# Performance work log

Measured on AMD Instinct MI355X. Metric: run time of the kernel, lower is better.

Reference implementation:

```python
import jax, jax.numpy as jnp
import numpy as np

LO = 30            # rollout horizon (hard-coded in SimCore)
AS_DIM = 400       # ssbm_actionstate_dim
HEAD = AS_DIM + 7  # per-player decoder width


def setup_inputs() -> dict:
    key = jax.random.key(0)
    ks = jax.random.split(key, 12)
    T, B, A, H = 128, 256, 64, 1024
    Nt, Ng = 6, 4
    Lu = T - 1 - LO
    s = 0.02
    return dict(
        observations=jax.random.uniform(ks[0], (T, B, 16), jnp.float32),
        actions=jax.random.normal(ks[1], (T, B, A), jnp.float32),
        beliefs=jax.random.normal(ks[2], (T, B, H), jnp.float32),
        w_ih=jax.random.normal(ks[3], (3 * H, A), jnp.float32) * s,
        w_hh=jax.random.normal(ks[4], (3 * H, H), jnp.float32) * s,
        b_ih=jnp.zeros((3 * H,), jnp.float32),
        b_hh=jnp.zeros((3 * H,), jnp.float32),
        pre_w1=jax.random.normal(ks[5], (64, H), jnp.float32) * s,
        pre_b1=jnp.zeros((64,), jnp.float32),
        pre_w2=jax.random.normal(ks[6], (H, 64), jnp.float32) * s,
        pre_b2=jnp.zeros((H,), jnp.float32),
        dec_w=jax.random.normal(ks[7], (2 * HEAD, H), jnp.float32) * s,
        dec_b=jnp.zeros((2 * HEAD,), jnp.float32),
        idx_i=jax.random.randint(ks[8], (Nt,), 0, Lu, dtype=jnp.int32),
        K=jax.random.randint(ks[9], (Nt, Ng), 0, LO, dtype=jnp.int32),
    )


def _bce_logits(x, t):
    # binary_cross_entropy_with_logits, elementwise
    return jax.nn.softplus(x) - x * t


def _player_loss(pred, tgt):
    # pred: [Nt,Ng,B,407] logits; tgt: [Nt,Ng,B,8] observation half
    # pytorch means are over everything except the Nt python loop -> mean over (Ng,B[,feat])
    logits = pred[..., :AS_DIM]
    cls = tgt[..., 0].astype(jnp.int32)                     # .long() of float target
    ce = -jnp.take_along_axis(jax.nn.log_softmax(logits, -1), cls[..., None], -1)[..., 0]
    loss = ce.mean(axis=(1, 2))
    loss = loss + ((pred[..., 400:402] - tgt[..., 1:3]) ** 2).mean(axis=(1, 2, 3))
    loss = loss + ((jax.nn.softplus(pred[..., 402:403]) - tgt[..., 3:4]) ** 2).mean(axis=(1, 2, 3))
    loss = loss + ((jax.nn.softplus(pred[..., 403:404]) - tgt[..., 4:5]) ** 2).mean(axis=(1, 2, 3))
    loss = loss + _bce_logits(pred[..., 404:405], tgt[..., 5:6]).mean(axis=(1, 2, 3))
    loss = loss + _bce_logits(pred[..., 405:406], tgt[..., 6:7]).mean(axis=(1, 2, 3))
    loss = loss + _bce_logits(pred[..., 406:407], tgt[..., 7:8]).mean(axis=(1, 2, 3))
    return loss  # [Nt]


def reference(observations, actions, beliefs, w_ih, w_hh, b_ih, b_hh,
              pre_w1, pre_b1, pre_w2, pre_b2, dec_w, dec_b, idx_i, K):
    def gru_cell(h, a):
        gi = a @ w_ih.T + b_ih              # [B,3H]
        gh = h @ w_hh.T + b_hh
        ir, iz, in_ = jnp.split(gi, 3, axis=-1)
        hr, hz, hn = jnp.split(gh, 3, axis=-1)
        r = jax.nn.sigmoid(ir + hr)
        z = jax.nn.sigmoid(iz + hz)
        n = jnp.tanh(in_ + r * hn)
        h_new = (1.0 - z) * n + z * h
        return h_new, h_new

    def rollout(i, k):
        h0 = beliefs[i]                                          # [B,H]
        acts = jax.lax.dynamic_slice_in_dim(actions, i, LO, axis=0)
        _, states = jax.lax.scan(gru_cell, h0, acts)             # [Lo,B,H]
        return states[k], observations[k + i + 1]                # [Ng,B,H],[Ng,B,16]

    states, obs = jax.vmap(rollout)(idx_i, K)                    # [Nt,Ng,B,H]

    # ResidualBlock: x + relu(relu(x W1^T + b1) W2^T + b2)
    h = jax.nn.relu(states @ pre_w1.T + pre_b1)
    x = states + jax.nn.relu(h @ pre_w2.T + pre_b2)

    logits = x @ dec_w.T + dec_b                                 # [Nt,Ng,B,814]
    agent, opponent = logits[..., :HEAD], logits[..., HEAD:]
    tgt_a, tgt_o = obs[..., :8], obs[..., 8:]

    loss = (_player_loss(agent, tgt_a) + _player_loss(opponent, tgt_o)).sum()
    return loss
```

## Files before the change

kernel.cpp:

```cpp
#include <hip/hip_runtime.h>
#include <hip/hip_bf16.h>
#include <hip/hip_fp8.h>

typedef __bf16 bf16;
typedef unsigned char u8;
typedef __attribute__((ext_vector_type(4))) __bf16 bf16x4;
typedef __attribute__((ext_vector_type(8))) __bf16 bf16x8;
typedef __attribute__((ext_vector_type(4))) float f32x4;

static __device__ __forceinline__ f32x4 MFMA16(bf16x8 a, bf16x8 b, f32x4 c) {
  return __builtin_amdgcn_mfma_f32_16x16x32_bf16(a, b, c, 0, 0, 0);
}
static __device__ __forceinline__ f32x4 MFMA8(long a, long b, f32x4 c) {
  return __builtin_amdgcn_mfma_f32_16x16x32_fp8_fp8(a, b, c, 0, 0, 0);
}

__device__ __forceinline__ float sigm(float x) { return 1.0f / (1.0f + __expf(-x)); }
__device__ __forceinline__ float softplus_(float x) {
  return fmaxf(x, 0.0f) + log1pf(__expf(-fabsf(x)));
}
__device__ __forceinline__ u8 to_fp8(float x) {
  __hip_fp8_e4m3 v(x);
  return (u8)v.__x;
}

__device__ __forceinline__ void gl16(const void* g, char* l) {
  __builtin_amdgcn_global_load_lds(
      (const __attribute__((address_space(1))) char*)g,
      (__attribute__((address_space(3))) char*)l, 16, 0, 0);
}

__global__ void k_prep(const float* __restrict__ whh, const float* __restrict__ wih,
                       const float* __restrict__ act, const float* __restrict__ w1,
                       const float* __restrict__ w2, const float* __restrict__ dw,
                       const float* __restrict__ beliefs, const int* __restrict__ idx_i,
                       u8* __restrict__ Wh8, bf16* __restrict__ Wib,
                       bf16* __restrict__ actb, bf16* __restrict__ w1b,
                       bf16* __restrict__ w2b, bf16* __restrict__ dwb,
                       bf16* __restrict__ hA, u8* __restrict__ hA8) {
  for (int q = blockIdx.x * blockDim.x + threadIdx.x; q < 1994240;
       q += gridDim.x * blockDim.x) {
    if (q < 814592) {
      const float* src;
      bf16* dst;
      int off;
      if (q < 49152)       { src = wih; dst = Wib;  off = q; }
      else if (q < 573440) { src = act; dst = actb; off = q - 49152; }
      else if (q < 589824) { src = w1;  dst = w1b;  off = q - 573440; }
      else if (q < 606208) { src = w2;  dst = w2b;  off = q - 589824; }
      else                 { src = dw;  dst = dwb;  off = q - 606208; }
      float4 v = *(const float4*)&src[(size_t)off << 2];
      bf16x4 o = {(bf16)v.x, (bf16)v.y, (bf16)v.z, (bf16)v.w};
      *(bf16x4*)&dst[(size_t)off << 2] = o;
    } else if (q < 1207808) {
      const int e = (q - 814592) << 2;
      const int n = e >> 18, rest = e & 262143;
      float4 v = *(const float4*)&beliefs[((size_t)idx_i[n] << 18) + rest];
      bf16x4 o = {(bf16)v.x, (bf16)v.y, (bf16)v.z, (bf16)v.w};
      *(bf16x4*)&hA[e] = o;
      unsigned w = (unsigned)to_fp8(v.x) | ((unsigned)to_fp8(v.y) << 8) |
                   ((unsigned)to_fp8(v.z) << 16) | ((unsigned)to_fp8(v.w) << 24);
      *(unsigned*)&hA8[e] = w;
    } else {
      const int off = q - 1207808;
      float4 v = *(const float4*)&whh[(size_t)off << 2];
      unsigned w = (unsigned)to_fp8(v.x) | ((unsigned)to_fp8(v.y) << 8) |
                   ((unsigned)to_fp8(v.z) << 16) | ((unsigned)to_fp8(v.w) << 24);
      *(unsigned*)&Wh8[(size_t)off << 2] = w;
    }
  }
}

__global__ __launch_bounds__(256, 2) void k_gru_step(
    const bf16* __restrict__ hin, const u8* __restrict__ hin8,
    bf16* __restrict__ hout, u8* __restrict__ hout8,
    const u8* __restrict__ Wh8, const bf16* __restrict__ Wib,
    const bf16* __restrict__ actb,
    const float* __restrict__ b_ih, const float* __restrict__ b_hh,
    const int* __restrict__ idx_i, const int* __restrict__ Kmat,
    bf16* __restrict__ states, int step) {
  const int pid = blockIdx.x;
  const int xcd = pid & 7;
  const int rg = xcd >> 2;
  const int cgp = xcd & 3;
  const int q = pid >> 3;
  const int mtl = q & 7;
  const int jtl = q >> 3;
  const int m0 = rg * 768 + mtl * 96;
  const int j0 = (cgp * 8 + jtl) * 32;

  {
    const int nlo = m0 >> 8, nhi = (m0 + 95) >> 8;
    int mk = max(max(Kmat[nlo * 4 + 0], Kmat[nlo * 4 + 1]),
                 max(Kmat[nlo * 4 + 2], Kmat[nlo * 4 + 3]));
    if (nhi != nlo)
      mk = max(mk, max(max(Kmat[nhi * 4 + 0], Kmat[nhi * 4 + 1]),
                       max(Kmat[nhi * 4 + 2], Kmat[nhi * 4 + 3])));
    if (step > mk) return;
  }

  const int tid = threadIdx.x, wave = tid >> 6, lane = tid & 63;
  const int l15 = lane & 15;
  const int kgrp = lane >> 4;
  const int wm = wave >> 1;
  const int wj = wave & 1;
  const int jlane = j0 + wj * 16 + l15;

  __shared__ alignas(16) char As[3 * 12288];
  __shared__ alignas(16) char Bs[3 * 12288];

  const int srow = lane >> 3;
  int a8off[3], b8off[3], aioff[3], bioff[3];
#pragma unroll
  for (int i = 0; i < 3; ++i) {
    const int r = wave * 24 + i * 8 + srow;
    const int grow = m0 + r;
    a8off[i] = grow * 1024 + ((((lane & 7) ^ ((r >> 1) & 7)) << 4));
    const int wr = (r >> 5) * 1024 + j0 + (r & 31);
    b8off[i] = wr * 1024 + ((((lane & 7) ^ ((r >> 1) & 7)) << 4));
    const int scol = (((lane & 7) ^ srow) << 3);
    const int np = grow >> 8;
    aioff[i] = ((idx_i[np] + step) * 256 + (grow & 255)) * 64 + scol;
    bioff[i] = wr * 64 + scol;
  }

  auto stage = [&](int buf, int slot) {
    char* ad = As + buf * 12288 + (wave * 24) * 128;
    char* bd = Bs + buf * 12288 + (wave * 24) * 128;
    if (slot < 8) {
#pragma unroll
      for (int i = 0; i < 3; ++i) {
        gl16(hin8 + a8off[i] + slot * 128, ad + i * 1024);
        gl16(Wh8 + b8off[i] + slot * 128, bd + i * 1024);
      }
    } else {
#pragma unroll
      for (int i = 0; i < 3; ++i) {
        gl16(actb + aioff[i], ad + i * 1024);
        gl16(Wib + bioff[i], bd + i * 1024);
      }
    }
  };

  f32x4 accR[3], accZ[3], accNh[3], accNi[3];
  const f32x4 zero = {0.f, 0.f, 0.f, 0.f};
#pragma unroll
  for (int f = 0; f < 3; ++f) { accR[f] = zero; accZ[f] = zero; accNh[f] = zero; accNi[f] = zero; }

  const float br = b_ih[jlane] + b_hh[jlane];
  const float bz = b_ih[1024 + jlane] + b_hh[1024 + jlane];
  const float bin = b_ih[2048 + jlane];
  const float bhn = b_hh[2048 + jlane];

  const int keyA = ((wm * 48 + l15) >> 1) & 7;
  const int keyB = ((wj * 16 + l15) >> 1) & 7;

  auto computeF8 = [&](int buf) {
    const char* ab = As + buf * 12288;
    const char* bb = Bs + buf * 12288;
    const int ra = wm * 48 + l15;
    const int rb = wj * 16 + l15;
#pragma unroll
    for (int kkI = 0; kkI < 4; ++kkI) {
      const int hi = kkI * 2 + (kgrp >> 1);
      const int lo = (kgrp & 1) << 3;
      const int offA = (((hi ^ keyA) << 4) | lo);
      const int offB = (((hi ^ keyB) << 4) | lo);
      long a0 = *(const long*)(ab + ra * 128 + offA);
      long a1 = *(const long*)(ab + (ra + 16) * 128 + offA);
      long a2 = *(const long*)(ab + (ra + 32) * 128 + offA);
      long b0 = *(const long*)(bb + rb * 128 + offB);
      long b1 = *(const long*)(bb + (rb + 32) * 128 + offB);
      long b2 = *(const long*)(bb + (rb + 64) * 128 + offB);
      accR[0] = MFMA8(a0, b0, accR[0]);
      accR[1] = MFMA8(a1, b0, accR[1]);
      accR[2] = MFMA8(a2, b0, accR[2]);
      accZ[0] = MFMA8(a0, b1, accZ[0]);
      accZ[1] = MFMA8(a1, b1, accZ[1]);
      accZ[2] = MFMA8(a2, b1, accZ[2]);
      accNh[0] = MFMA8(a0, b2, accNh[0]);
      accNh[1] = MFMA8(a1, b2, accNh[1]);
      accNh[2] = MFMA8(a2, b2, accNh[2]);
    }
  };

  auto computeGi = [&]() {
    const char* ab = As + 2 * 12288;
    const char* bb = Bs + 2 * 12288;
#pragma unroll
    for (int kkI = 0; kkI < 2; ++kkI) {
      const int kbyte = (((kkI << 5) + (kgrp << 3)) << 1) ^ ((l15 & 7) << 4);
      bf16x8 a0 = *(const bf16x8*)(ab + (wm * 48 + l15) * 128 + kbyte);
      bf16x8 a1 = *(const bf16x8*)(ab + (wm * 48 + 16 + l15) * 128 + kbyte);
      bf16x8 a2 = *(const bf16x8*)(ab + (wm * 48 + 32 + l15) * 128 + kbyte);
      bf16x8 b_r = *(const bf16x8*)(bb + (wj * 16 + l15) * 128 + kbyte);
      bf16x8 b_z = *(const bf16x8*)(bb + (32 + wj * 16 + l15) * 128 + kbyte);
      bf16x8 b_n = *(const bf16x8*)(bb + (64 + wj * 16 + l15) * 128 + kbyte);
      accR[0] = MFMA16(a0, b_r, accR[0]);
      accR[1] = MFMA16(a1, b_r, accR[1]);
      accR[2] = MFMA16(a2, b_r, accR[2]);
      accZ[0] = MFMA16(a0, b_z, accZ[0]);
      accZ[1] = MFMA16(a1, b_z, accZ[1]);
      accZ[2] = MFMA16(a2, b_z, accZ[2]);
      accNi[0] = MFMA16(a0, b_n, accNi[0]);
      accNi[1] = MFMA16(a1, b_n, accNi[1]);
      accNi[2] = MFMA16(a2, b_n, accNi[2]);
    }
  };

  stage(0, 0);
  stage(1, 1);

  uint2 hpreg[3];

#pragma unroll
  for (int t = 0; t < 9; ++t) {
    if (t < 7) stage((t + 2) % 3, t + 2);
    if (t == 6) {
#pragma unroll
      for (int it2 = 0; it2 < 3; ++it2) {
        const int u = it2 * 256 + tid;
        const int row = u >> 3, c = u & 7;
        hpreg[it2] = *(const uint2*)(hin + (size_t)(m0 + row) * 1024 + j0 + c * 4);
      }
    }
    if (t <= 5)       asm volatile("s_waitcnt vmcnt(12)" ::: "memory");
    else if (t == 6)  asm volatile("s_waitcnt vmcnt(15)" ::: "memory");
    else if (t == 7)  asm volatile("s_waitcnt vmcnt(9)" ::: "memory");
    else              asm volatile("s_waitcnt vmcnt(3)" ::: "memory");
    __builtin_amdgcn_s_barrier();
    if (t == 8) computeGi();
    else        computeF8(t % 3);
    __builtin_amdgcn_sched_barrier(0);
    __builtin_amdgcn_s_barrier();
  }

  asm volatile("s_waitcnt vmcnt(0)" ::: "memory");
  bf16* Hp = (bf16*)As;
  bf16* Hn = (bf16*)Bs;
  u8* Hn8 = (u8*)(As + 12288);

#pragma unroll
  for (int it2 = 0; it2 < 3; ++it2) {
    const int u = it2 * 256 + tid;
    const int row = u >> 3, c = u & 7;
    *(uint2*)&Hp[row * 40 + c * 4] = hpreg[it2];
  }
  __syncthreads();

#pragma unroll
  for (int mf = 0; mf < 3; ++mf) {
#pragma unroll
    for (int ii = 0; ii < 4; ++ii) {
      const int ml = wm * 48 + mf * 16 + kgrp * 4 + ii;
      const int jl = wj * 16 + l15;
      float hp = (float)Hp[ml * 40 + jl];
      float rg2 = sigm(accR[mf][ii] + br);
      float zg = sigm(accZ[mf][ii] + bz);
      float ng = tanhf(accNi[mf][ii] + bin + rg2 * (accNh[mf][ii] + bhn));
      float hnew = (1.0f - zg) * ng + zg * hp;
      Hn[ml * 40 + jl] = (bf16)hnew;
      Hn8[ml * 40 + jl] = to_fp8(hnew);
    }
  }
  __syncthreads();

#pragma unroll
  for (int it2 = 0; it2 < 3; ++it2) {
    const int u = it2 * 256 + tid;
    const int row = u >> 3, c = u & 7;
    const int m = m0 + row;
    uint2 v = *(const uint2*)&Hn[row * 40 + c * 4];
    *(uint2*)&hout[(size_t)m * 1024 + j0 + c * 4] = v;
    if (c < 8) {
    }
    const int n = m >> 8;
    const int b = m & 255;
#pragma unroll
    for (int g = 0; g < 4; ++g) {
      if (Kmat[n * 4 + g] == step)
        *(uint2*)&states[((size_t)(n * 4 + g) * 256 + b) * 1024 + j0 + c * 4] = v;
    }
  }
#pragma unroll
  for (int it2 = 0; it2 < 3; ++it2) {
    const int u = it2 * 256 + tid;
    const int row = u >> 3, c = u & 7;
    *(unsigned*)&hout8[(size_t)(m0 + row) * 1024 + j0 + c * 4] =
        *(const unsigned*)&Hn8[row * 40 + c * 4];
  }
}

template <int EPI, int SWZ>
__global__ __launch_bounds__(256) void k_gemm_epi(
    const bf16* __restrict__ A, const bf16* __restrict__ W, int K, int Nreal, int ld_out,
    const float* __restrict__ bias, const bf16* __restrict__ resid,
    float* __restrict__ outF, bf16* __restrict__ outB) {
  int mt, jt;
  if (SWZ) {
    const int lin = blockIdx.x;
    const int x = lin & 7, k = lin >> 3;
    mt = 12 * x + k % 12;
    jt = k / 12;
  } else {
    mt = blockIdx.x;
    jt = blockIdx.y;
  }
  const int m0 = mt * 64;
  const int j0 = jt * 64;
  const int tid = threadIdx.x, wave = tid >> 6, lane = tid & 63;
  __shared__ alignas(16) bf16 Al[64][72];
  __shared__ alignas(16) bf16 Wl[64][72];

  f32x4 acc[4];
  const f32x4 zero = {0.f, 0.f, 0.f, 0.f};
#pragma unroll
  for (int f = 0; f < 4; ++f) acc[f] = zero;

  const int r = tid >> 3, c8 = (tid & 7) << 3;
  const int arow = wave * 16 + (lane & 15);
  const int koff = (lane >> 4) << 3;

  for (int kb = 0; kb < K; kb += 64) {
    *(bf16x8*)&Al[r][c8]      = *(const bf16x8*)&A[(size_t)(m0 + r) * K + kb + c8];
    *(bf16x8*)&Al[r + 32][c8] = *(const bf16x8*)&A[(size_t)(m0 + r + 32) * K + kb + c8];
    int jr = j0 + r;      if (jr >= Nreal) jr = Nreal - 1;
    int jr2 = j0 + r + 32; if (jr2 >= Nreal) jr2 = Nreal - 1;
    *(bf16x8*)&Wl[r][c8]      = *(const bf16x8*)&W[(size_t)jr * K + kb + c8];
    *(bf16x8*)&Wl[r + 32][c8] = *(const bf16x8*)&W[(size_t)jr2 * K + kb + c8];
    __syncthreads();
#pragma unroll
    for (int kk = 0; kk < 64; kk += 32) {
      bf16x8 av = *(const bf16x8*)&Al[arow][kk + koff];
#pragma unroll
      for (int nf = 0; nf < 4; ++nf) {
        acc[nf] = MFMA16(av, *(const bf16x8*)&Wl[nf * 16 + (lane & 15)][kk + koff], acc[nf]);
      }
    }
    __syncthreads();
  }

#pragma unroll
  for (int nf = 0; nf < 4; ++nf) {
    int j = j0 + nf * 16 + (lane & 15);
    float bj = (j < Nreal) ? bias[j] : 0.f;
#pragma unroll
    for (int i = 0; i < 4; ++i) {
      int m = m0 + wave * 16 + ((lane >> 4) << 2) + i;
      float v = acc[nf][i] + bj;
      if (EPI == 0) {
        outB[(size_t)m * ld_out + j] = (bf16)fmaxf(v, 0.f);
      } else if (EPI == 1) {
        v = fmaxf(v, 0.f) + (float)resid[(size_t)m * ld_out + j];
        outB[(size_t)m * ld_out + j] = (bf16)v;
      } else {
        if (j < Nreal) outF[(size_t)m * ld_out + j] = v;
      }
    }
  }
}

__global__ __launch_bounds__(256) void k_loss_wave(
    const float* __restrict__ logits, const float* __restrict__ obs,
    const int* __restrict__ idx_i, const int* __restrict__ Kmat,
    float* __restrict__ partials) {
  const int gw = blockIdx.x * 4 + (threadIdx.x >> 6);
  const int lane = threadIdx.x & 63;
  const int row = gw >> 1, p = gw & 1;
  const int n = row >> 10, g = (row >> 8) & 3, b = row & 255;
  const int i = idx_i[n], k = Kmat[n * 4 + g];
  const float* Lp = logits + (size_t)row * 814 + p * 407;
  const float* tg = obs + ((size_t)(k + i + 1) * 256 + b) * 16 + p * 8;

  float v[7];
#pragma unroll
  for (int it = 0; it < 7; ++it) {
    const int c = lane + it * 64;
    v[it] = (c < 400) ? Lp[c] : -1e30f;
  }
  float mx = fmaxf(fmaxf(fmaxf(v[0], v[1]), fmaxf(v[2], v[3])),
                   fmaxf(fmaxf(v[4], v[5]), v[6]));
#pragma unroll
  for (int s = 32; s; s >>= 1) mx = fmaxf(mx, __shfl_xor(mx, s));
  float se = 0.f;
#pragma unroll
  for (int it = 0; it < 7; ++it) {
    const int c = lane + it * 64;
    se += (c < 400) ? __expf(v[it] - mx) : 0.f;
  }
#pragma unroll
  for (int s = 32; s; s >>= 1) se += __shfl_xor(se, s);

  if (lane == 0) {
    const int cls = (int)tg[0];
    float val = mx + logf(se) - Lp[cls];
    const float d0 = Lp[400] - tg[1], d1 = Lp[401] - tg[2];
    val += 0.5f * (d0 * d0 + d1 * d1);
    const float s2 = softplus_(Lp[402]) - tg[3]; val += s2 * s2;
    const float s3 = softplus_(Lp[403]) - tg[4]; val += s3 * s3;
    val += softplus_(Lp[404]) - Lp[404] * tg[5];
    val += softplus_(Lp[405]) - Lp[405] * tg[6];
    val += softplus_(Lp[406]) - Lp[406] * tg[7];
    partials[gw] = val * (1.0f / 1024.0f);
  }
}

__global__ void k_reduce_final(const float* __restrict__ partials, float* __restrict__ out) {
  __shared__ float s[256];
  float v = 0.f;
  for (int i = threadIdx.x; i < 12288; i += 256) v += partials[i];
  s[threadIdx.x] = v;
  __syncthreads();
  for (int st = 128; st; st >>= 1) {
    if (threadIdx.x < st) s[threadIdx.x] += s[threadIdx.x + st];
    __syncthreads();
  }
  if (threadIdx.x == 0) out[0] = s[0];
}


extern "C" void kernel_launch(void* const* d_in, const int* in_sizes, int n_in,
                              void* d_out, int out_size, void* d_ws, size_t ws_size,
                              hipStream_t stream) {
  const float* obs      = (const float*)d_in[0];
  const float* actions  = (const float*)d_in[1];
  const float* beliefs  = (const float*)d_in[2];
  const float* w_ih     = (const float*)d_in[3];
  const float* w_hh     = (const float*)d_in[4];
  const float* b_ih     = (const float*)d_in[5];
  const float* b_hh     = (const float*)d_in[6];
  const float* pre_w1   = (const float*)d_in[7];
  const float* pre_b1   = (const float*)d_in[8];
  const float* pre_w2   = (const float*)d_in[9];
  const float* pre_b2   = (const float*)d_in[10];
  const float* dec_w    = (const float*)d_in[11];
  const float* dec_b    = (const float*)d_in[12];
  const int*   idx_i    = (const int*)d_in[13];
  const int*   Kmat     = (const int*)d_in[14];
  float* outF = (float*)d_out;

  char* p = (char*)d_ws;
  auto carve = [&](size_t bytes) {
    char* q = p;
    p += (bytes + 255) & ~(size_t)255;
    return q;
  };
  u8*   Wh8     = (u8*)carve(3072u * 1024u);
  bf16* Wib     = (bf16*)carve(3072u * 64u * 2u);
  bf16* actb    = (bf16*)carve(128u * 256u * 64u * 2u);
  bf16* preW1b  = (bf16*)carve(64u * 1024u * 2u);
  bf16* preW2b  = (bf16*)carve(1024u * 64u * 2u);
  bf16* decWb   = (bf16*)carve(814u * 1024u * 2u);
  bf16* hA      = (bf16*)carve(1536u * 1024u * 2u);
  bf16* hB      = (bf16*)carve(1536u * 1024u * 2u);
  u8*   hA8     = (u8*)carve(1536u * 1024u);
  u8*   hB8     = (u8*)carve(1536u * 1024u);
  bf16* states  = (bf16*)carve(6144u * 1024u * 2u);
  bf16* h1      = (bf16*)carve(6144u * 64u * 2u);
  bf16* xbuf    = (bf16*)carve(6144u * 1024u * 2u);
  float* logits = (float*)carve((size_t)6144u * 814u * 4u);
  float* partials = (float*)carve(12288u * 4u);

  k_prep<<<2048, 256, 0, stream>>>(w_hh, w_ih, actions, pre_w1, pre_w2, dec_w,
                                   beliefs, idx_i, Wh8, Wib, actb, preW1b, preW2b,
                                   decWb, hA, hA8);

  for (int t = 0; t < 30; ++t) {
    const bf16* hi = (t & 1) ? hB : hA;
    bf16* ho = (t & 1) ? hA : hB;
    const u8* hi8 = (t & 1) ? hB8 : hA8;
    u8* ho8 = (t & 1) ? hA8 : hB8;
    k_gru_step<<<512, 256, 0, stream>>>(hi, hi8, ho, ho8, Wh8, Wib, actb,
                                        b_ih, b_hh, idx_i, Kmat, states, t);
  }

  k_gemm_epi<0, 0><<<dim3(96, 1), 256, 0, stream>>>(states, preW1b, 1024, 64, 64,
                                                    pre_b1, nullptr, nullptr, h1);
  k_gemm_epi<1, 1><<<1536, 256, 0, stream>>>(h1, preW2b, 64, 1024, 1024,
                                             pre_b2, states, nullptr, xbuf);
  k_gemm_epi<2, 1><<<1248, 256, 0, stream>>>(xbuf, decWb, 1024, 814, 814,
                                             dec_b, nullptr, logits, nullptr);

  k_loss_wave<<<3072, 256, 0, stream>>>(logits, obs, idx_i, Kmat, partials);
  k_reduce_final<<<1, 256, 0, stream>>>(partials, outF);
}
```

Before: 566.7 us.

## Fuse GRU rollout steps into one persistent cooperative kernel with per-tile flags

Replaces the 30 per-step GRU kernel launches with one cooperative persistent kernel in which each block loops over steps. Blocks synchronise through per-row-tile completion counters in global memory instead of grid-wide kernel boundaries. The bf16 hidden-state copy is dropped: the previous h is read back from the fp8 buffer, and every step writes to its own slot in a history buffer, which removes the ping-pong and cuts traffic. The costs are spin-wait polling, lower precision in the z*h term, and a bounded spin guard that could silently break out early.

```diff
diff --git a/kernel.cpp b/kernel.cpp
--- a/kernel.cpp
+++ b/kernel.cpp
@@ -22,6 +22,11 @@
 __device__ __forceinline__ u8 to_fp8(float x) {
   __hip_fp8_e4m3 v(x);
   return (u8)v.__x;
+}
+__device__ __forceinline__ float from_fp8(u8 b) {
+  __hip_fp8_e4m3 v;
+  v.__x = b;
+  return (float)v;
 }
 
 __device__ __forceinline__ void gl16(const void* g, char* l) {
@@ -37,7 +42,7 @@
                        u8* __restrict__ Wh8, bf16* __restrict__ Wib,
                        bf16* __restrict__ actb, bf16* __restrict__ w1b,
                        bf16* __restrict__ w2b, bf16* __restrict__ dwb,
-                       bf16* __restrict__ hA, u8* __restrict__ hA8) {
+                       u8* __restrict__ hbuf) {
   for (int q = blockIdx.x * blockDim.x + threadIdx.x; q < 1994240;
        q += gridDim.x * blockDim.x) {
     if (q < 814592) {
@@ -56,11 +61,9 @@
       const int e = (q - 814592) << 2;
       const int n = e >> 18, rest = e & 262143;
       float4 v = *(const float4*)&beliefs[((size_t)idx_i[n] << 18) + rest];
-      bf16x4 o = {(bf16)v.x, (bf16)v.y, (bf16)v.z, (bf16)v.w};
-      *(bf16x4*)&hA[e] = o;
       unsigned w = (unsigned)to_fp8(v.x) | ((unsigned)to_fp8(v.y) << 8) |
                    ((unsigned)to_fp8(v.z) << 16) | ((unsigned)to_fp8(v.w) << 24);
-      *(unsigned*)&hA8[e] = w;
+      *(unsigned*)&hbuf[e] = w;
     } else {
       const int off = q - 1207808;
       float4 v = *(const float4*)&whh[(size_t)off << 2];
@@ -71,14 +74,13 @@
   }
 }
 
-__global__ __launch_bounds__(256, 2) void k_gru_step(
-    const bf16* __restrict__ hin, const u8* __restrict__ hin8,
-    bf16* __restrict__ hout, u8* __restrict__ hout8,
+__global__ __launch_bounds__(256, 2) void k_gru_all(
+    u8* __restrict__ hbuf,
     const u8* __restrict__ Wh8, const bf16* __restrict__ Wib,
     const bf16* __restrict__ actb,
     const float* __restrict__ b_ih, const float* __restrict__ b_hh,
     const int* __restrict__ idx_i, const int* __restrict__ Kmat,
-    bf16* __restrict__ states, int step) {
+    bf16* __restrict__ states, int* __restrict__ done) {
   const int pid = blockIdx.x;
   const int xcd = pid & 7;
   const int rg = xcd >> 2;
@@ -88,15 +90,16 @@
   const int jtl = q >> 3;
   const int m0 = rg * 768 + mtl * 96;
   const int j0 = (cgp * 8 + jtl) * 32;
-
+  const int mtIdx = rg * 8 + mtl;
+
+  int mk;
   {
     const int nlo = m0 >> 8, nhi = (m0 + 95) >> 8;
-    int mk = max(max(Kmat[nlo * 4 + 0], Kmat[nlo * 4 + 1]),
-                 max(Kmat[nlo * 4 + 2], Kmat[nlo * 4 + 3]));
+    mk = max(max(Kmat[nlo * 4 + 0], Kmat[nlo * 4 + 1]),
+             max(Kmat[nlo * 4 + 2], Kmat[nlo * 4 + 3]));
     if (nhi != nlo)
       mk = max(mk, max(max(Kmat[nhi * 4 + 0], Kmat[nhi * 4 + 1]),
                        max(Kmat[nhi * 4 + 2], Kmat[nhi * 4 + 3])));
-    if (step > mk) return;
   }
 
   const int tid = threadIdx.x, wave = tid >> 6, lane = tid & 63;
@@ -110,7 +113,7 @@
   __shared__ alignas(16) char Bs[3 * 12288];
 
   const int srow = lane >> 3;
-  int a8off[3], b8off[3], aioff[3], bioff[3];
+  int a8off[3], b8off[3], aibase[3], bioff[3];
 #pragma unroll
   for (int i = 0; i < 3; ++i) {
     const int r = wave * 24 + i * 8 + srow;
@@ -120,32 +123,9 @@
     b8off[i] = wr * 1024 + ((((lane & 7) ^ ((r >> 1) & 7)) << 4));
     const int scol = (((lane & 7) ^ srow) << 3);
     const int np = grow >> 8;
-    aioff[i] = ((idx_i[np] + step) * 256 + (grow & 255)) * 64 + scol;
+    aibase[i] = (idx_i[np] * 256 + (grow & 255)) * 64 + scol;
     bioff[i] = wr * 64 + scol;
   }
-
-  auto stage = [&](int buf, int slot) {
-    char* ad = As + buf * 12288 + (wave * 24) * 128;
-    char* bd = Bs + buf * 12288 + (wave * 24) * 128;
-    if (slot < 8) {
-#pragma unroll
-      for (int i = 0; i < 3; ++i) {
-        gl16(hin8 + a8off[i] + slot * 128, ad + i * 1024);
-        gl16(Wh8 + b8off[i] + slot * 128, bd + i * 1024);
-      }
-    } else {
-#pragma unroll
-      for (int i = 0; i < 3; ++i) {
-        gl16(actb + aioff[i], ad + i * 1024);
-        gl16(Wib + bioff[i], bd + i * 1024);
-      }
-    }
-  };
-
-  f32x4 accR[3], accZ[3], accNh[3], accNi[3];
-  const f32x4 zero = {0.f, 0.f, 0.f, 0.f};
-#pragma unroll
-  for (int f = 0; f < 3; ++f) { accR[f] = zero; accZ[f] = zero; accNh[f] = zero; accNi[f] = zero; }
 
   const float br = b_ih[jlane] + b_hh[jlane];
   const float bz = b_ih[1024 + jlane] + b_hh[1024 + jlane];
@@ -155,139 +135,180 @@
   const int keyA = ((wm * 48 + l15) >> 1) & 7;
   const int keyB = ((wj * 16 + l15) >> 1) & 7;
 
-  auto computeF8 = [&](int buf) {
-    const char* ab = As + buf * 12288;
-    const char* bb = Bs + buf * 12288;
-    const int ra = wm * 48 + l15;
-    const int rb = wj * 16 + l15;
-#pragma unroll
-    for (int kkI = 0; kkI < 4; ++kkI) {
-      const int hi = kkI * 2 + (kgrp >> 1);
-      const int lo = (kgrp & 1) << 3;
-      const int offA = (((hi ^ keyA) << 4) | lo);
-      const int offB = (((hi ^ keyB) << 4) | lo);
-      long a0 = *(const long*)(ab + ra * 128 + offA);
-      long a1 = *(const long*)(ab + (ra + 16) * 128 + offA);
-      long a2 = *(const long*)(ab + (ra + 32) * 128 + offA);
-      long b0 = *(const long*)(bb + rb * 128 + offB);
-      long b1 = *(const long*)(bb + (rb + 32) * 128 + offB);
-      long b2 = *(const long*)(bb + (rb + 64) * 128 + offB);
-      accR[0] = MFMA8(a0, b0, accR[0]);
-      accR[1] = MFMA8(a1, b0, accR[1]);
-      accR[2] = MFMA8(a2, b0, accR[2]);
-      accZ[0] = MFMA8(a0, b1, accZ[0]);
-      accZ[1] = MFMA8(a1, b1, accZ[1]);
-      accZ[2] = MFMA8(a2, b1, accZ[2]);
-      accNh[0] = MFMA8(a0, b2, accNh[0]);
-      accNh[1] = MFMA8(a1, b2, accNh[1]);
-      accNh[2] = MFMA8(a2, b2, accNh[2]);
-    }
-  };
-
-  auto computeGi = [&]() {
-    const char* ab = As + 2 * 12288;
-    const char* bb = Bs + 2 * 12288;
-#pragma unroll
-    for (int kkI = 0; kkI < 2; ++kkI) {
-      const int kbyte = (((kkI << 5) + (kgrp << 3)) << 1) ^ ((l15 & 7) << 4);
-      bf16x8 a0 = *(const bf16x8*)(ab + (wm * 48 + l15) * 128 + kbyte);
-      bf16x8 a1 = *(const bf16x8*)(ab + (wm * 48 + 16 + l15) * 128 + kbyte);
-      bf16x8 a2 = *(const bf16x8*)(ab + (wm * 48 + 32 + l15) * 128 + kbyte);
-      bf16x8 b_r = *(const bf16x8*)(bb + (wj * 16 + l15) * 128 + kbyte);
-      bf16x8 b_z = *(const bf16x8*)(bb + (32 + wj * 16 + l15) * 128 + kbyte);
-      bf16x8 b_n = *(const bf16x8*)(bb + (64 + wj * 16 + l15) * 128 + kbyte);
-      accR[0] = MFMA16(a0, b_r, accR[0]);
-      accR[1] = MFMA16(a1, b_r, accR[1]);
-      accR[2] = MFMA16(a2, b_r, accR[2]);
-      accZ[0] = MFMA16(a0, b_z, accZ[0]);
-      accZ[1] = MFMA16(a1, b_z, accZ[1]);
-      accZ[2] = MFMA16(a2, b_z, accZ[2]);
-      accNi[0] = MFMA16(a0, b_n, accNi[0]);
-      accNi[1] = MFMA16(a1, b_n, accNi[1]);
-      accNi[2] = MFMA16(a2, b_n, accNi[2]);
-    }
-  };
-
-  stage(0, 0);
-  stage(1, 1);
-
-  uint2 hpreg[3];
-
-#pragma unroll
-  for (int t = 0; t < 9; ++t) {
-    if (t < 7) stage((t + 2) % 3, t + 2);
-    if (t == 6) {
-#pragma unroll
-      for (int it2 = 0; it2 < 3; ++it2) {
-        const int u = it2 * 256 + tid;
-        const int row = u >> 3, c = u & 7;
-        hpreg[it2] = *(const uint2*)(hin + (size_t)(m0 + row) * 1024 + j0 + c * 4);
-      }
-    }
-    if (t <= 5)       asm volatile("s_waitcnt vmcnt(12)" ::: "memory");
-    else if (t == 6)  asm volatile("s_waitcnt vmcnt(15)" ::: "memory");
-    else if (t == 7)  asm volatile("s_waitcnt vmcnt(9)" ::: "memory");
-    else              asm volatile("s_waitcnt vmcnt(3)" ::: "memory");
-    __builtin_amdgcn_s_barrier();
-    if (t == 8) computeGi();
-    else        computeF8(t % 3);
-    __builtin_amdgcn_sched_barrier(0);
-    __builtin_amdgcn_s_barrier();
-  }
-
-  asm volatile("s_waitcnt vmcnt(0)" ::: "memory");
-  bf16* Hp = (bf16*)As;
-  bf16* Hn = (bf16*)Bs;
-  u8* Hn8 = (u8*)(As + 12288);
-
-#pragma unroll
-  for (int it2 = 0; it2 < 3; ++it2) {
-    const int u = it2 * 256 + tid;
-    const int row = u >> 3, c = u & 7;
-    *(uint2*)&Hp[row * 40 + c * 4] = hpreg[it2];
-  }
-  __syncthreads();
-
-#pragma unroll
-  for (int mf = 0; mf < 3; ++mf) {
-#pragma unroll
-    for (int ii = 0; ii < 4; ++ii) {
-      const int ml = wm * 48 + mf * 16 + kgrp * 4 + ii;
-      const int jl = wj * 16 + l15;
-      float hp = (float)Hp[ml * 40 + jl];
-      float rg2 = sigm(accR[mf][ii] + br);
-      float zg = sigm(accZ[mf][ii] + bz);
-      float ng = tanhf(accNi[mf][ii] + bin + rg2 * (accNh[mf][ii] + bhn));
-      float hnew = (1.0f - zg) * ng + zg * hp;
-      Hn[ml * 40 + jl] = (bf16)hnew;
-      Hn8[ml * 40 + jl] = to_fp8(hnew);
-    }
-  }
-  __syncthreads();
-
-#pragma unroll
-  for (int it2 = 0; it2 < 3; ++it2) {
-    const int u = it2 * 256 + tid;
-    const int row = u >> 3, c = u & 7;
-    const int m = m0 + row;
-    uint2 v = *(const uint2*)&Hn[row * 40 + c * 4];
-    *(uint2*)&hout[(size_t)m * 1024 + j0 + c * 4] = v;
-    if (c < 8) {
-    }
-    const int n = m >> 8;
-    const int b = m & 255;
-#pragma unroll
-    for (int g = 0; g < 4; ++g) {
-      if (Kmat[n * 4 + g] == step)
-        *(uint2*)&states[((size_t)(n * 4 + g) * 256 + b) * 1024 + j0 + c * 4] = v;
-    }
-  }
-#pragma unroll
-  for (int it2 = 0; it2 < 3; ++it2) {
-    const int u = it2 * 256 + tid;
-    const int row = u >> 3, c = u & 7;
-    *(unsigned*)&hout8[(size_t)(m0 + row) * 1024 + j0 + c * 4] =
-        *(const unsigned*)&Hn8[row * 40 + c * 4];
+  f32x4 accR[3], accZ[3], accNh[3], accNi[3];
+  const f32x4 zero = {0.f, 0.f, 0.f, 0.f};
+
+  for (int s = 0; s <= mk; ++s) {
+    const u8* hs = hbuf + (size_t)s * 1572864u;
+    u8* hn = hbuf + (size_t)(s + 1) * 1572864u;
+
+    if (s > 0) {
+      if (tid == 0) {
+        int guard = 0;
+        while (__hip_atomic_load(&done[(s - 1) * 16 + mtIdx], __ATOMIC_RELAXED,
+                                 __HIP_MEMORY_SCOPE_AGENT) < 32) {
+          __builtin_amdgcn_s_sleep(1);
+          if (++guard > (1 << 22)) break;
+        }
+      }
+      __syncthreads();
+    }
+
+    auto stage = [&](int buf, int slot) {
+      char* ad = As + buf * 12288 + (wave * 24) * 128;
+      char* bd = Bs + buf * 12288 + (wave * 24) * 128;
+      if (slot < 8) {
+#pragma unroll
+        for (int i = 0; i < 3; ++i) {
+          gl16(hs + a8off[i] + slot * 128, ad + i * 1024);
+          gl16(Wh8 + b8off[i] + slot * 128, bd + i * 1024);
+        }
+      } else {
+#pragma unroll
+        for (int i = 0; i < 3; ++i) {
+          gl16(actb + aibase[i] + s * 16384, ad + i * 1024);
+          gl16(Wib + bioff[i], bd + i * 1024);
+        }
+      }
+    };
+
+#pragma unroll
+    for (int f = 0; f < 3; ++f) { accR[f] = zero; accZ[f] = zero; accNh[f] = zero; accNi[f] = zero; }
+
+    auto computeF8 = [&](int buf) {
+      const char* ab = As + buf * 12288;
+      const char* bb = Bs + buf * 12288;
+      const int ra = wm * 48 + l15;
+      const int rb = wj * 16 + l15;
+#pragma unroll
+      for (int kkI = 0; kkI < 4; ++kkI) {
+        const int hi = kkI * 2 + (kgrp >> 1);
+        const int lo = (kgrp & 1) << 3;
+        const int offA = (((hi ^ keyA) << 4) | lo);
+        const int offB = (((hi ^ keyB) << 4) | lo);
+        long a0 = *(const long*)(ab + ra * 128 + offA);
+        long a1 = *(const long*)(ab + (ra + 16) * 128 + offA);
+        long a2 = *(const long*)(ab + (ra + 32) * 128 + offA);
+        long b0 = *(const long*)(bb + rb * 128 + offB);
+        long b1 = *(const long*)(bb + (rb + 32) * 128 + offB);
+        long b2 = *(const long*)(bb + (rb + 64) * 128 + offB);
+        accR[0] = MFMA8(a0, b0, accR[0]);
+        accR[1] = MFMA8(a1, b0, accR[1]);
+        accR[2] = MFMA8(a2, b0, accR[2]);
+        accZ[0] = MFMA8(a0, b1, accZ[0]);
+        accZ[1] = MFMA8(a1, b1, accZ[1]);
+        accZ[2] = MFMA8(a2, b1, accZ[2]);
+        accNh[0] = MFMA8(a0, b2, accNh[0]);
+        accNh[1] = MFMA8(a1, b2, accNh[1]);
+        accNh[2] = MFMA8(a2, b2, accNh[2]);
+      }
+    };
+
+    auto computeGi = [&]() {
+      const char* ab = As + 2 * 12288;
+      const char* bb = Bs + 2 * 12288;
+#pragma unroll
+      for (int kkI = 0; kkI < 2; ++kkI) {
+        const int kbyte = (((kkI << 5) + (kgrp << 3)) << 1) ^ ((l15 & 7) << 4);
+        bf16x8 a0 = *(const bf16x8*)(ab + (wm * 48 + l15) * 128 + kbyte);
+        bf16x8 a1 = *(const bf16x8*)(ab + (wm * 48 + 16 + l15) * 128 + kbyte);
+        bf16x8 a2 = *(const bf16x8*)(ab + (wm * 48 + 32 + l15) * 128 + kbyte);
+        bf16x8 b_r = *(const bf16x8*)(bb + (wj * 16 + l15) * 128 + kbyte);
+        bf16x8 b_z = *(const bf16x8*)(bb + (32 + wj * 16 + l15) * 128 + kbyte);
+        bf16x8 b_n = *(const bf16x8*)(bb + (64 + wj * 16 + l15) * 128 + kbyte);
+        accR[0] = MFMA16(a0, b_r, accR[0]);
+        accR[1] = MFMA16(a1, b_r, accR[1]);
+        accR[2] = MFMA16(a2, b_r, accR[2]);
+        accZ[0] = MFMA16(a0, b_z, accZ[0]);
+        accZ[1] = MFMA16(a1, b_z, accZ[1]);
+        accZ[2] = MFMA16(a2, b_z, accZ[2]);
+        accNi[0] = MFMA16(a0, b_n, accNi[0]);
+        accNi[1] = MFMA16(a1, b_n, accNi[1]);
+        accNi[2] = MFMA16(a2, b_n, accNi[2]);
+      }
+    };
+
+    stage(0, 0);
+    stage(1, 1);
+
+    unsigned hp8reg[3];
+
+#pragma unroll
+    for (int t = 0; t < 9; ++t) {
+      if (t < 7) stage((t + 2) % 3, t + 2);
+      if (t == 6) {
+#pragma unroll
+        for (int it2 = 0; it2 < 3; ++it2) {
+          const int u = it2 * 256 + tid;
+          const int row = u >> 3, c = u & 7;
+          hp8reg[it2] = *(const unsigned*)(hs + (size_t)(m0 + row) * 1024 + j0 + c * 4);
+        }
+      }
+      if (t <= 5)       asm volatile("s_waitcnt vmcnt(12)" ::: "memory");
+      else if (t == 6)  asm volatile("s_waitcnt vmcnt(15)" ::: "memory");
+      else if (t == 7)  asm volatile("s_waitcnt vmcnt(9)" ::: "memory");
+      else              asm volatile("s_waitcnt vmcnt(3)" ::: "memory");
+      __builtin_amdgcn_s_barrier();
+      if (t == 8) computeGi();
+      else        computeF8(t % 3);
+      __builtin_amdgcn_sched_barrier(0);
+      __builtin_amdgcn_s_barrier();
+    }
+
+    asm volatile("s_waitcnt vmcnt(0)" ::: "memory");
+    u8* Hp8 = (u8*)As;
+    bf16* Hn = (bf16*)Bs;
+    u8* Hn8 = (u8*)(As + 12288);
+
+#pragma unroll
+    for (int it2 = 0; it2 < 3; ++it2) {
+      const int u = it2 * 256 + tid;
+      const int row = u >> 3, c = u & 7;
+      *(unsigned*)&Hp8[row * 40 + c * 4] = hp8reg[it2];
+    }
+    __syncthreads();
+
+#pragma unroll
+    for (int mf = 0; mf < 3; ++mf) {
+#pragma unroll
+      for (int ii = 0; ii < 4; ++ii) {
+        const int ml = wm * 48 + mf * 16 + kgrp * 4 + ii;
+        const int jl = wj * 16 + l15;
+        float hp = from_fp8(Hp8[ml * 40 + jl]);
+        float rg2 = sigm(accR[mf][ii] + br);
+        float zg = sigm(accZ[mf][ii] + bz);
+        float ng = tanhf(accNi[mf][ii] + bin + rg2 * (accNh[mf][ii] + bhn));
+        float hnew = (1.0f - zg) * ng + zg * hp;
+        Hn[ml * 40 + jl] = (bf16)hnew;
+        Hn8[ml * 40 + jl] = to_fp8(hnew);
+      }
+    }
+    __syncthreads();
+
+#pragma unroll
+    for (int it2 = 0; it2 < 3; ++it2) {
+      const int u = it2 * 256 + tid;
+      const int row = u >> 3, c = u & 7;
+      const int m = m0 + row;
+      *(unsigned*)&hn[(size_t)m * 1024 + j0 + c * 4] =
+          *(const unsigned*)&Hn8[row * 40 + c * 4];
+      const int n = m >> 8;
+      const int b = m & 255;
+      uint2 v = *(const uint2*)&Hn[row * 40 + c * 4];
+#pragma unroll
+      for (int g = 0; g < 4; ++g) {
+        if (Kmat[n * 4 + g] == s)
+          *(uint2*)&states[((size_t)(n * 4 + g) * 256 + b) * 1024 + j0 + c * 4] = v;
+      }
+    }
+
+    asm volatile("s_waitcnt vmcnt(0)" ::: "memory");
+    __syncthreads();
+    if (tid == 0) {
+      __threadfence();
+      __hip_atomic_fetch_add(&done[s * 16 + mtIdx], 1, __ATOMIC_RELEASE,
+                             __HIP_MEMORY_SCOPE_AGENT);
+    }
   }
 }
 
@@ -451,27 +472,25 @@
   bf16* preW1b  = (bf16*)carve(64u * 1024u * 2u);
   bf16* preW2b  = (bf16*)carve(1024u * 64u * 2u);
   bf16* decWb   = (bf16*)carve(814u * 1024u * 2u);
-  bf16* hA      = (bf16*)carve(1536u * 1024u * 2u);
-  bf16* hB      = (bf16*)carve(1536u * 1024u * 2u);
-  u8*   hA8     = (u8*)carve(1536u * 1024u);
-  u8*   hB8     = (u8*)carve(1536u * 1024u);
+  u8*   hbuf    = (u8*)carve(31u * 1536u * 1024u);
   bf16* states  = (bf16*)carve(6144u * 1024u * 2u);
   bf16* h1      = (bf16*)carve(6144u * 64u * 2u);
   bf16* xbuf    = (bf16*)carve(6144u * 1024u * 2u);
   float* logits = (float*)carve((size_t)6144u * 814u * 4u);
   float* partials = (float*)carve(12288u * 4u);
+  int*  done    = (int*)carve(480u * 4u);
+
+  hipMemsetAsync(done, 0, 480u * sizeof(int), stream);
 
   k_prep<<<2048, 256, 0, stream>>>(w_hh, w_ih, actions, pre_w1, pre_w2, dec_w,
                                    beliefs, idx_i, Wh8, Wib, actb, preW1b, preW2b,
-                                   decWb, hA, hA8);
-
-  for (int t = 0; t < 30; ++t) {
-    const bf16* hi = (t & 1) ? hB : hA;
-    bf16* ho = (t & 1) ? hA : hB;
-    const u8* hi8 = (t & 1) ? hB8 : hA8;
-    u8* ho8 = (t & 1) ? hA8 : hB8;
-    k_gru_step<<<512, 256, 0, stream>>>(hi, hi8, ho, ho8, Wh8, Wib, actb,
-                                        b_ih, b_hh, idx_i, Kmat, states, t);
+                                   decWb, hbuf);
+
+  {
+    void* args[] = {(void*)&hbuf, (void*)&Wh8, (void*)&Wib, (void*)&actb,
+                    (void*)&b_ih, (void*)&b_hh, (void*)&idx_i, (void*)&Kmat,
+                    (void*)&states, (void*)&done};
+    hipLaunchCooperativeKernel((const void*)k_gru_all, dim3(512), dim3(256), args, 0, stream);
   }
 
   k_gemm_epi<0, 0><<<dim3(96, 1), 256, 0, stream>>>(states, preW1b, 1024, 64, 64,
```

Result: slower. 1.505 ms (+165.5%).
